# Performance work log

Hardware: AMD Instinct MI355X
Metric: run time of the kernel (lower is better)

Reference implementation:

```python
import jax, jax.numpy as jnp
import numpy as np

DIM = 1024
HEADS = 16
HEAD_DIM = DIM // HEADS
B, NQ, NK = 2, 2048, 2048


def setup_inputs() -> dict:
    key = jax.random.key(0)
    ks = jax.random.split(key, 8)
    s = 1.0 / np.sqrt(DIM)
    return {
        "query": jax.random.normal(ks[0], (B, NQ, DIM), jnp.float32),
        "key": jax.random.normal(ks[1], (B, NK, DIM), jnp.float32),
        "value": jax.random.normal(ks[2], (B, NK, DIM), jnp.float32),
        "qpos": jnp.zeros((B, NQ), jnp.int32),
        "kpos": jnp.zeros((B, NK), jnp.int32),
        "Wq": jax.random.normal(ks[3], (DIM, DIM), jnp.float32) * s,
        "Wk": jax.random.normal(ks[4], (DIM, DIM), jnp.float32) * s,
        "Wv": jax.random.normal(ks[5], (DIM, DIM), jnp.float32) * s,
        "Wo": jax.random.normal(ks[6], (DIM, DIM), jnp.float32) * s,
        "bo": jax.random.normal(ks[7], (DIM,), jnp.float32) * s,
    }


def reference(query, key, value, qpos, kpos, Wq, Wk, Wv, Wo, bo):
    # torch nn.Linear: y = x @ W.T (qkv_bias=False)
    Bq, Nq, C = query.shape
    Nk = key.shape[1]
    scale = HEAD_DIM ** -0.5
    # project and split heads: (B, H, N, Dh)
    q = (query @ Wq.T).reshape(Bq, Nq, HEADS, HEAD_DIM).transpose(0, 2, 1, 3)
    k = (key @ Wk.T).reshape(Bq, Nk, HEADS, HEAD_DIM).transpose(0, 2, 1, 3)
    v = (value @ Wv.T).reshape(Bq, Nk, HEADS, HEAD_DIM).transpose(0, 2, 1, 3)
    # rope is None, qk_norm False -> plain softmax attention
    attn = jnp.einsum("bhqd,bhkd->bhqk", q, k) * scale  # [B,H,Nq,Nk]
    attn = jax.nn.softmax(attn, axis=-1)
    x = jnp.einsum("bhqk,bhkd->bhqd", attn, v)
    x = x.transpose(0, 2, 1, 3).reshape(Bq, Nq, C)
    return x @ Wo.T + bo
```

## Files before the change

### kernel.cpp

```cpp
#include <hip/hip_runtime.h>
#include <hip/hip_bf16.h>
#include <stdint.h>

typedef __bf16 bf16_t;
typedef __bf16 bf16x4 __attribute__((ext_vector_type(4)));
typedef __bf16 bf16x8 __attribute__((ext_vector_type(8)));
typedef float  f32x4  __attribute__((ext_vector_type(4)));
typedef unsigned u32x2 __attribute__((ext_vector_type(2)));

#define MFMA16(a,b,c) __builtin_amdgcn_mfma_f32_16x16x32_bf16((a),(b),(c),0,0,0)

static constexpr int DIM = 1024, HEADS = 16, HD = 64, NB = 2, NQ = 2048, NKK = 2048;
static constexpr int MROWS = NB * NQ;
static constexpr float SCALE_Q = 0.18033688011112042f;

__global__ void cvt_all(const float* __restrict__ q, const float* __restrict__ k,
                        const float* __restrict__ v, const float* __restrict__ wq,
                        const float* __restrict__ wk, const float* __restrict__ wv,
                        const float* __restrict__ wo,
                        bf16_t* qb, bf16_t* kb, bf16_t* vb,
                        bf16_t* wqb, bf16_t* wkb, bf16_t* wvb, bf16_t* wob) {
  const int seg = blockIdx.y;
  const float* src; bf16_t* dst;
  size_t base;
  if (seg < 12) {
    int t = seg >> 2;
    src = t == 0 ? q : t == 1 ? k : v;
    dst = t == 0 ? qb : t == 1 ? kb : vb;
    base = (size_t)(seg & 3) * 262144;
  } else {
    int t = seg - 12;
    src = t == 0 ? wq : t == 1 ? wk : t == 2 ? wv : wo;
    dst = t == 0 ? wqb : t == 1 ? wkb : t == 2 ? wvb : wob;
    base = 0;
  }
  size_t i = base + blockIdx.x * 256 + threadIdx.x;
  float4 val = reinterpret_cast<const float4*>(src)[i];
  bf16x4 o;
  o[0] = (bf16_t)val.x; o[1] = (bf16_t)val.y; o[2] = (bf16_t)val.z; o[3] = (bf16_t)val.w;
  *reinterpret_cast<bf16x4*>(dst + i * 4) = o;
}

template<int ROWS, int TPB = 256>
__device__ __forceinline__ void stage_swz(const bf16_t* gbase, int gstride, bf16_t* lds, int tid) {
#pragma unroll
  for (int c = 0; c < ROWS * 8 / TPB; ++c) {
    int p = c * TPB + tid;
    int r = p >> 3, x = p & 7;
    const bf16_t* src = gbase + (size_t)r * gstride + ((x ^ (r & 7)) << 3);
    __builtin_amdgcn_global_load_lds(
        (const __attribute__((address_space(1))) void*)src,
        (__attribute__((address_space(3))) void*)(lds + (p << 3)),
        16, 0, 0);
  }
}

__device__ __forceinline__ bf16x8 lds_read8_swz(const bf16_t* lds, int row, int chunk) {
  int sc = chunk ^ (row & 7);
  return *reinterpret_cast<const bf16x8*>(lds + row * 64 + (sc << 3));
}

__device__ __forceinline__ unsigned cvtpk_bf16(float lo, float hi) {
  unsigned r;
  asm("v_cvt_pk_bf16_f32 %0, %1, %2" : "=v"(r) : "v"(lo), "v"(hi));
  return r;
}

__global__ __launch_bounds__(256) void gemm_qkv(const bf16_t* __restrict__ qb,
                                                const bf16_t* __restrict__ kb,
                                                const bf16_t* __restrict__ vb,
                                                const bf16_t* __restrict__ Wq,
                                                const bf16_t* __restrict__ Wk,
                                                const bf16_t* __restrict__ Wv,
                                                bf16_t* __restrict__ Qp,
                                                bf16_t* __restrict__ Kp,
                                                bf16_t* __restrict__ Vt) {
  constexpr int K = DIM, N = DIM;
  __shared__ __align__(16) bf16_t As[128 * 64];
  __shared__ __align__(16) bf16_t Bs[128 * 64];
  const int tid = threadIdx.x;
  const int lane = tid & 63, wid = tid >> 6;
  const int l15 = lane & 15, lg = lane >> 4;
  const int wr = wid >> 1, wc = wid & 1;
  const int bn = blockIdx.x, bm = blockIdx.y;
  const int sel = bn >> 3, bnl = bn & 7;

  const bf16_t* A  = sel == 0 ? qb : sel == 1 ? kb : vb;
  const bf16_t* Bt = sel == 0 ? Wq : sel == 1 ? Wk : Wv;
  const bf16_t* Abase = A + (size_t)(bm * 128) * K;
  const bf16_t* Bbase = Bt + (size_t)(bnl * 128) * K;

  f32x4 acc[4][4];
#pragma unroll
  for (int m = 0; m < 4; ++m)
#pragma unroll
    for (int n = 0; n < 4; ++n) acc[m][n] = (f32x4){0.f, 0.f, 0.f, 0.f};

  for (int k0 = 0; k0 < K; k0 += 64) {
    __syncthreads();
    stage_swz<128>(Abase + k0, K, As, tid);
    stage_swz<128>(Bbase + k0, K, Bs, tid);
    __syncthreads();
#pragma unroll
    for (int kk = 0; kk < 2; ++kk) {
      bf16x8 af[4], bfr[4];
#pragma unroll
      for (int m = 0; m < 4; ++m) af[m] = lds_read8_swz(As, wr * 64 + m * 16 + l15, kk * 4 + lg);
#pragma unroll
      for (int n = 0; n < 4; ++n) bfr[n] = lds_read8_swz(Bs, wc * 64 + n * 16 + l15, kk * 4 + lg);
#pragma unroll
      for (int m = 0; m < 4; ++m)
#pragma unroll
        for (int n = 0; n < 4; ++n)
          acc[m][n] = MFMA16(af[m], bfr[n], acc[m][n]);
    }
  }

  if (sel == 2) {
#pragma unroll
    for (int m = 0; m < 4; ++m) {
      int row0 = bm * 128 + wr * 64 + m * 16 + lg * 4;
      int bb = row0 >> 11, kv = row0 & 2047;
#pragma unroll
      for (int n = 0; n < 4; ++n) {
        int col = bnl * 128 + wc * 64 + n * 16 + l15;
        int hh = col >> 6, dd = col & 63;
        bf16x4 pk;
#pragma unroll
        for (int j = 0; j < 4; ++j) pk[j] = (bf16_t)acc[m][n][j];
        *reinterpret_cast<bf16x4*>(Vt + (((size_t)((bb * 16 + hh) * 64 + dd)) << 11) + kv) = pk;
      }
    }
  } else {
    bf16_t* Cout = sel == 0 ? Qp : Kp;
    const float scale = sel == 0 ? SCALE_Q : 1.0f;
#pragma unroll
    for (int m = 0; m < 4; ++m)
#pragma unroll
      for (int n = 0; n < 4; ++n)
#pragma unroll
        for (int j = 0; j < 4; ++j) {
          int row = bm * 128 + wr * 64 + m * 16 + lg * 4 + j;
          int col = bnl * 128 + wc * 64 + n * 16 + l15;
          Cout[(size_t)row * N + col] = (bf16_t)(acc[m][n][j] * scale);
        }
  }
}

__global__ __launch_bounds__(256) void gemm_out(const bf16_t* __restrict__ A,
                                                const bf16_t* __restrict__ Bt,
                                                float* __restrict__ Cout,
                                                const float* __restrict__ bias) {
  constexpr int K = DIM, N = DIM;
  __shared__ __align__(16) bf16_t As[128 * 64];
  __shared__ __align__(16) bf16_t Bs[128 * 64];
  const int tid = threadIdx.x;
  const int lane = tid & 63, wid = tid >> 6;
  const int l15 = lane & 15, lg = lane >> 4;
  const int wr = wid >> 1, wc = wid & 1;
  const int bn = blockIdx.x, bm = blockIdx.y;

  const bf16_t* Abase = A + (size_t)(bm * 128) * K;
  const bf16_t* Bbase = Bt + (size_t)(bn * 128) * K;

  f32x4 acc[4][4];
#pragma unroll
  for (int m = 0; m < 4; ++m)
#pragma unroll
    for (int n = 0; n < 4; ++n) acc[m][n] = (f32x4){0.f, 0.f, 0.f, 0.f};

  for (int k0 = 0; k0 < K; k0 += 64) {
    __syncthreads();
    stage_swz<128>(Abase + k0, K, As, tid);
    stage_swz<128>(Bbase + k0, K, Bs, tid);
    __syncthreads();
#pragma unroll
    for (int kk = 0; kk < 2; ++kk) {
      bf16x8 af[4], bfr[4];
#pragma unroll
      for (int m = 0; m < 4; ++m) af[m] = lds_read8_swz(As, wr * 64 + m * 16 + l15, kk * 4 + lg);
#pragma unroll
      for (int n = 0; n < 4; ++n) bfr[n] = lds_read8_swz(Bs, wc * 64 + n * 16 + l15, kk * 4 + lg);
#pragma unroll
      for (int m = 0; m < 4; ++m)
#pragma unroll
        for (int n = 0; n < 4; ++n)
          acc[m][n] = MFMA16(af[m], bfr[n], acc[m][n]);
    }
  }

#pragma unroll
  for (int m = 0; m < 4; ++m)
#pragma unroll
    for (int n = 0; n < 4; ++n)
#pragma unroll
      for (int j = 0; j < 4; ++j) {
        int row = bm * 128 + wr * 64 + m * 16 + lg * 4 + j;
        int col = bn * 128 + wc * 64 + n * 16 + l15;
        Cout[(size_t)row * N + col] = acc[m][n][j] + bias[col];
      }
}

__global__ __launch_bounds__(512) void attn_fused(const bf16_t* __restrict__ Qp,
                                                  const bf16_t* __restrict__ Kp,
                                                  const bf16_t* __restrict__ Vt,
                                                  bf16_t* __restrict__ Xa) {
  __shared__ __align__(16) bf16_t Ks[2][64 * 64];
  __shared__ __align__(16) bf16_t Vs[2][64 * 64];
  __shared__ __align__(16) bf16_t Ps[8][16 * 64];
  const int tid = threadIdx.x;
  const int lane = tid & 63, wid = tid >> 6;
  const int l15 = lane & 15, lg = lane >> 4;
  const int rot = (l15 & 7) * 8;

  int id = blockIdx.x + 16 * (blockIdx.y + 16 * blockIdx.z);
  int swz = (id & 7) * 64 + (id >> 3);
  const int bx = swz & 15, h = (swz >> 4) & 15, b = swz >> 8;
  const int q0 = bx * 128;

  const bf16_t* qbase = Qp + ((size_t)(b * NQ + q0)) * DIM + h * HD;
  const bf16_t* kbase = Kp + ((size_t)b * NKK) * DIM + h * HD;
  const bf16_t* vbase = Vt + ((size_t)((b * HEADS + h) * HD)) * NKK;

  stage_swz<128, 512>(qbase, DIM, &Ks[0][0], tid);
  __syncthreads();
  bf16x8 qf[2];
  qf[0] = lds_read8_swz(&Ks[0][0], wid * 16 + l15, lg);
  qf[1] = lds_read8_swz(&Ks[0][0], wid * 16 + l15, 4 + lg);
  __syncthreads();

  float m_ = -1e30f, l_ = 0.f;
  f32x4 o[4];
#pragma unroll
  for (int n = 0; n < 4; ++n) o[n] = (f32x4){0.f, 0.f, 0.f, 0.f};

  constexpr int NT = NKK / 64;

#define QK_TILE(kl, sdst)                                              \
  do {                                                                 \
    __builtin_amdgcn_s_setprio(1);                                     \
    _Pragma("unroll")                                                  \
    for (int tt = 0; tt < 4; ++tt) {                                   \
      bf16x8 kf0 = lds_read8_swz((kl), tt * 16 + l15, lg);             \
      bf16x8 kf1 = lds_read8_swz((kl), tt * 16 + l15, 4 + lg);         \
      f32x4 a = (f32x4){0.f, 0.f, 0.f, 0.f};                           \
      a = MFMA16(kf0, qf[0], a);                                       \
      a = MFMA16(kf1, qf[1], a);                                       \
      (sdst)[tt] = a;                                                  \
    }                                                                  \
    __builtin_amdgcn_s_setprio(0);                                     \
  } while (0)

  stage_swz<64, 512>(kbase, DIM, &Ks[0][0], tid);
  stage_swz<64, 512>(vbase, NKK, &Vs[0][0], tid);
  asm volatile("s_waitcnt vmcnt(0)" ::: "memory");
  __builtin_amdgcn_s_barrier();
  __builtin_amdgcn_sched_barrier(0);
  f32x4 scur[4];
  QK_TILE(&Ks[0][0], scur);
  stage_swz<64, 512>(kbase + (size_t)64 * DIM, DIM, &Ks[1][0], tid);

  for (int t = 0; t < NT; ++t) {
    __builtin_amdgcn_s_barrier();
    __builtin_amdgcn_sched_barrier(0);

    if (t + 1 < NT) stage_swz<64, 512>(vbase + (t + 1) * 64, NKK, &Vs[(t + 1) & 1][0], tid);
    if (t + 2 < NT) stage_swz<64, 512>(kbase + (size_t)(t + 2) * 64 * DIM, DIM, &Ks[t & 1][0], tid);

    if (t + 2 < NT)      asm volatile("s_waitcnt vmcnt(2)" ::: "memory");
    else if (t + 1 < NT) asm volatile("s_waitcnt vmcnt(1)" ::: "memory");
    else                 asm volatile("s_waitcnt vmcnt(0)" ::: "memory");
    __builtin_amdgcn_s_barrier();
    __builtin_amdgcn_sched_barrier(0);

    f32x4 snx[4];
    if (t + 1 < NT) QK_TILE(&Ks[(t + 1) & 1][0], snx);

    float rm = scur[0][0];
#pragma unroll
    for (int tt = 0; tt < 4; ++tt)
#pragma unroll
      for (int j = 0; j < 4; ++j) rm = fmaxf(rm, scur[tt][j]);
    rm = fmaxf(rm, __shfl_xor(rm, 16));
    rm = fmaxf(rm, __shfl_xor(rm, 32));
    if (!__all(rm <= m_ + 8.f)) {
      float mn = fmaxf(m_, rm);
      float al = exp2f(m_ - mn);
      m_ = mn;
      l_ *= al;
#pragma unroll
      for (int n = 0; n < 4; ++n)
#pragma unroll
        for (int j = 0; j < 4; ++j) o[n][j] *= al;
    }
    float rs = 0.f;
#pragma unroll
    for (int tt = 0; tt < 4; ++tt)
#pragma unroll
      for (int j = 0; j < 4; ++j) {
        float p = exp2f(scur[tt][j] - m_);
        scur[tt][j] = p;
        rs += p;
      }
    rs += __shfl_xor(rs, 16);
    rs += __shfl_xor(rs, 32);
    l_ += rs;

    bf16_t* Pw = &Ps[wid][0];
#pragma unroll
    for (int tt = 0; tt < 4; ++tt) {
      unsigned w0 = cvtpk_bf16(scur[tt][0], scur[tt][1]);
      unsigned w1 = cvtpk_bf16(scur[tt][2], scur[tt][3]);
      int col = (16 * tt + 4 * lg + rot) & 63;
      u32x2 pk2 = {w0, w1};
      *reinterpret_cast<u32x2*>(reinterpret_cast<char*>(Pw) + l15 * 128 + col * 2) = pk2;
    }
    asm volatile("s_waitcnt lgkmcnt(0)" ::: "memory");
    bf16x8 pf[2];
#pragma unroll
    for (int kt = 0; kt < 2; ++kt) {
      int col = (32 * kt + 8 * lg + rot) & 63;
      pf[kt] = *reinterpret_cast<const bf16x8*>(reinterpret_cast<const char*>(Pw) + l15 * 128 + col * 2);
    }

    const bf16_t* vl = &Vs[t & 1][0];
    __builtin_amdgcn_s_setprio(1);
#pragma unroll
    for (int n = 0; n < 4; ++n) {
#pragma unroll
      for (int kt = 0; kt < 2; ++kt) {
        bf16x8 vf = lds_read8_swz(vl, n * 16 + l15, 4 * kt + lg);
        o[n] = MFMA16(vf, pf[kt], o[n]);
      }
    }
    __builtin_amdgcn_s_setprio(0);

    if (t + 1 < NT) {
#pragma unroll
      for (int tt = 0; tt < 4; ++tt) scur[tt] = snx[tt];
    }
  }
#undef QK_TILE

  float inv = 1.f / l_;
  int q = q0 + wid * 16 + l15;
  bf16_t* ob = Xa + ((size_t)(b * NQ + q)) * DIM + h * HD;
#pragma unroll
  for (int n = 0; n < 4; ++n) {
    bf16x4 pk;
#pragma unroll
    for (int j = 0; j < 4; ++j) pk[j] = (bf16_t)(o[n][j] * inv);
    *reinterpret_cast<bf16x4*>(ob + n * 16 + 4 * lg) = pk;
  }
}

extern "C" void kernel_launch(void* const* d_in, const int* in_sizes, int n_in,
                              void* d_out, int out_size, void* d_ws, size_t ws_size,
                              hipStream_t stream) {
  (void)in_sizes; (void)n_in; (void)out_size; (void)ws_size;
  const float* q  = (const float*)d_in[0];
  const float* k  = (const float*)d_in[1];
  const float* v  = (const float*)d_in[2];
  const float* Wq = (const float*)d_in[5];
  const float* Wk = (const float*)d_in[6];
  const float* Wv = (const float*)d_in[7];
  const float* Wo = (const float*)d_in[8];
  const float* bo = (const float*)d_in[9];
  float* out = (float*)d_out;

  bf16_t* ws = (bf16_t*)d_ws;
  const size_t SZ_IN = (size_t)MROWS * DIM;
  const size_t SZ_W  = (size_t)DIM * DIM;
  bf16_t* qb  = ws;
  bf16_t* kb  = qb  + SZ_IN;
  bf16_t* vb  = kb  + SZ_IN;
  bf16_t* wqb = vb  + SZ_IN;
  bf16_t* wkb = wqb + SZ_W;
  bf16_t* wvb = wkb + SZ_W;
  bf16_t* wob = wvb + SZ_W;
  bf16_t* Qp  = wob + SZ_W;
  bf16_t* Kp  = Qp  + SZ_IN;
  bf16_t* Vtp = Kp  + SZ_IN;
  bf16_t* Xa  = qb;

  cvt_all<<<dim3(1024, 16), 256, 0, stream>>>(q, k, v, Wq, Wk, Wv, Wo,
                                              qb, kb, vb, wqb, wkb, wvb, wob);

  gemm_qkv<<<dim3(24, MROWS / 128), 256, 0, stream>>>(qb, kb, vb, wqb, wkb, wvb,
                                                      Qp, Kp, Vtp);

  attn_fused<<<dim3(NQ / 128, HEADS, NB), 512, 0, stream>>>(Qp, Kp, Vtp, Xa);

  gemm_out<<<dim3(DIM / 128, MROWS / 128), 256, 0, stream>>>(Xa, wob, out, bo);
}
```

Measured before the change: 157.8 us.

## Load K fragments directly from global into registers, drop K shared-memory staging

The K tile is no longer staged through LDS. Each lane now loads its K MFMA fragments straight from global memory into registers, prefetching the next tile while the current one is processed. The Q staging buffer reuses the V LDS area, and the cross-iteration QK software pipeline with its explicit vmcnt waits is replaced by a single __syncthreads per tile. This is meant to cut LDS traffic and footprint, but every wave (8 per block) now redundantly reads the same K tile from global memory and exposes more load latency, because QK now runs in the same iteration as the softmax.

```diff
diff --git a/kernel.cpp b/kernel.cpp
--- a/kernel.cpp
+++ b/kernel.cpp
@@ -205,7 +205,6 @@
                                                   const bf16_t* __restrict__ Kp,
                                                   const bf16_t* __restrict__ Vt,
                                                   bf16_t* __restrict__ Xa) {
-  __shared__ __align__(16) bf16_t Ks[2][64 * 64];
   __shared__ __align__(16) bf16_t Vs[2][64 * 64];
   __shared__ __align__(16) bf16_t Ps[8][16 * 64];
   const int tid = threadIdx.x;
@@ -222,11 +221,13 @@
   const bf16_t* kbase = Kp + ((size_t)b * NKK) * DIM + h * HD;
   const bf16_t* vbase = Vt + ((size_t)((b * HEADS + h) * HD)) * NKK;
 
-  stage_swz<128, 512>(qbase, DIM, &Ks[0][0], tid);
+  const bf16_t* klane = kbase + (size_t)l15 * DIM + lg * 8;
+
+  stage_swz<128, 512>(qbase, DIM, &Vs[0][0], tid);
   __syncthreads();
   bf16x8 qf[2];
-  qf[0] = lds_read8_swz(&Ks[0][0], wid * 16 + l15, lg);
-  qf[1] = lds_read8_swz(&Ks[0][0], wid * 16 + l15, 4 + lg);
+  qf[0] = lds_read8_swz(&Vs[0][0], wid * 16 + l15, lg);
+  qf[1] = lds_read8_swz(&Vs[0][0], wid * 16 + l15, 4 + lg);
   __syncthreads();
 
   float m_ = -1e30f, l_ = 0.f;
@@ -236,45 +237,38 @@
 
   constexpr int NT = NKK / 64;
 
-#define QK_TILE(kl, sdst)                                              \
-  do {                                                                 \
-    __builtin_amdgcn_s_setprio(1);                                     \
-    _Pragma("unroll")                                                  \
-    for (int tt = 0; tt < 4; ++tt) {                                   \
-      bf16x8 kf0 = lds_read8_swz((kl), tt * 16 + l15, lg);             \
-      bf16x8 kf1 = lds_read8_swz((kl), tt * 16 + l15, 4 + lg);         \
-      f32x4 a = (f32x4){0.f, 0.f, 0.f, 0.f};                           \
-      a = MFMA16(kf0, qf[0], a);                                       \
-      a = MFMA16(kf1, qf[1], a);                                       \
-      (sdst)[tt] = a;                                                  \
-    }                                                                  \
-    __builtin_amdgcn_s_setprio(0);                                     \
-  } while (0)
-
-  stage_swz<64, 512>(kbase, DIM, &Ks[0][0], tid);
   stage_swz<64, 512>(vbase, NKK, &Vs[0][0], tid);
-  asm volatile("s_waitcnt vmcnt(0)" ::: "memory");
-  __builtin_amdgcn_s_barrier();
-  __builtin_amdgcn_sched_barrier(0);
-  f32x4 scur[4];
-  QK_TILE(&Ks[0][0], scur);
-  stage_swz<64, 512>(kbase + (size_t)64 * DIM, DIM, &Ks[1][0], tid);
+  bf16x8 kf[8];
+#pragma unroll
+  for (int tt = 0; tt < 4; ++tt)
+#pragma unroll
+    for (int hf = 0; hf < 2; ++hf)
+      kf[tt * 2 + hf] = *reinterpret_cast<const bf16x8*>(
+          klane + (size_t)(16 * tt) * DIM + hf * 32);
+  __syncthreads();
 
   for (int t = 0; t < NT; ++t) {
-    __builtin_amdgcn_s_barrier();
-    __builtin_amdgcn_sched_barrier(0);
-
-    if (t + 1 < NT) stage_swz<64, 512>(vbase + (t + 1) * 64, NKK, &Vs[(t + 1) & 1][0], tid);
-    if (t + 2 < NT) stage_swz<64, 512>(kbase + (size_t)(t + 2) * 64 * DIM, DIM, &Ks[t & 1][0], tid);
-
-    if (t + 2 < NT)      asm volatile("s_waitcnt vmcnt(2)" ::: "memory");
-    else if (t + 1 < NT) asm volatile("s_waitcnt vmcnt(1)" ::: "memory");
-    else                 asm volatile("s_waitcnt vmcnt(0)" ::: "memory");
-    __builtin_amdgcn_s_barrier();
-    __builtin_amdgcn_sched_barrier(0);
-
-    f32x4 snx[4];
-    if (t + 1 < NT) QK_TILE(&Ks[(t + 1) & 1][0], snx);
+    f32x4 scur[4];
+    __builtin_amdgcn_s_setprio(1);
+#pragma unroll
+    for (int tt = 0; tt < 4; ++tt) {
+      f32x4 a = (f32x4){0.f, 0.f, 0.f, 0.f};
+      a = MFMA16(kf[tt * 2 + 0], qf[0], a);
+      a = MFMA16(kf[tt * 2 + 1], qf[1], a);
+      scur[tt] = a;
+    }
+    __builtin_amdgcn_s_setprio(0);
+
+    if (t + 1 < NT) {
+      const bf16_t* kn = klane + (size_t)(t + 1) * 64 * DIM;
+#pragma unroll
+      for (int tt = 0; tt < 4; ++tt)
+#pragma unroll
+        for (int hf = 0; hf < 2; ++hf)
+          kf[tt * 2 + hf] = *reinterpret_cast<const bf16x8*>(
+              kn + (size_t)(16 * tt) * DIM + hf * 32);
+      stage_swz<64, 512>(vbase + (t + 1) * 64, NKK, &Vs[(t + 1) & 1][0], tid);
+    }
 
     float rm = scur[0][0];
 #pragma unroll
@@ -335,12 +329,8 @@
     }
     __builtin_amdgcn_s_setprio(0);
 
-    if (t + 1 < NT) {
-#pragma unroll
-      for (int tt = 0; tt < 4; ++tt) scur[tt] = snx[tt];
-    }
-  }
-#undef QK_TILE
+    __syncthreads();
+  }
 
   float inv = 1.f / l_;
   int q = q0 + wid * 16 + l15;
```

Result: slower. 224.3 us (+42.1%).
